# Kernel tuning notes

Hardware: AMD Instinct MI355X
Metric: run time of the kernel (lower is better)

Reference implementation:

```python
import jax, jax.numpy as jnp
import numpy as np

NUM_SLOTS = 2048
LATENT_DIM = 512
EPS = 1e-12  # torch F.normalize clamps norm at eps


def _l2_normalize(x, axis):
    n = jnp.linalg.norm(x, axis=axis, keepdims=True)
    return x / jnp.maximum(n, EPS)


def setup_inputs() -> dict:
    key = jax.random.key(0)
    k_z, k_m = jax.random.split(key)
    z = jax.random.normal(k_z, (65536, LATENT_DIM), dtype=jnp.float32)
    memory = jax.random.normal(k_m, (NUM_SLOTS, LATENT_DIM), dtype=jnp.float32)
    return {"z": z, "memory": memory}


def reference(z, memory):
    # cosine-similarity attention over memory slots
    z_norm = _l2_normalize(z, axis=1)          # [B, D]
    mem_norm = _l2_normalize(memory, axis=1)   # [N, D]
    attn = jax.nn.softmax(z_norm @ mem_norm.T, axis=1)  # [B, N]
    z_hat = attn @ memory                      # [B, D] (unnormalized memory, as in source)
    return (z_hat, attn)
```

## Files before the change

### kernel.cpp

```cpp
#include <hip/hip_runtime.h>

#define NSLOTS 2048
#define DIM    512

typedef __bf16 bf16x8 __attribute__((ext_vector_type(8)));
typedef float  f32x4  __attribute__((ext_vector_type(4)));
typedef unsigned short us4 __attribute__((ext_vector_type(4)));
typedef unsigned short us8 __attribute__((ext_vector_type(8)));

typedef const __attribute__((address_space(1))) unsigned* gp_t;
typedef __attribute__((address_space(3))) unsigned* sp_t;

__device__ __forceinline__ void gl16(const void* g, void* l) {
    __builtin_amdgcn_global_load_lds((gp_t)g, (sp_t)l, 16, 0, 0);
}

__device__ __forceinline__ unsigned short f2bf(float f) {
    unsigned u = __builtin_bit_cast(unsigned, f);
    u = (u + 0x7FFFu + ((u >> 16) & 1u)) >> 16;
    return (unsigned short)u;
}
__device__ __forceinline__ float bf2f(unsigned short u) {
    unsigned v = ((unsigned)u) << 16;
    return __builtin_bit_cast(float, v);
}

__global__ __launch_bounds__(512) void prep_kernel(const float* __restrict__ mem,
                                                   unsigned short* __restrict__ memN,
                                                   unsigned short* __restrict__ memT) {
    __shared__ unsigned short T[32][516];
    const int tid = threadIdx.x;
    const int sl  = tid >> 4;
    const int c16 = tid & 15;
    const int n   = blockIdx.x * 32 + sl;
    const f32x4* row = (const f32x4*)(mem + (size_t)n * DIM);
    f32x4 v[8];
    float s = 0.f;
    #pragma unroll
    for (int j = 0; j < 8; ++j) {
        v[j] = row[c16*8 + j];
        s += v[j][0]*v[j][0] + v[j][1]*v[j][1] + v[j][2]*v[j][2] + v[j][3]*v[j][3];
    }
    #pragma unroll
    for (int off = 1; off < 16; off <<= 1) s += __shfl_xor(s, off);
    const float rn = 1.0f / fmaxf(sqrtf(s), 1e-12f);
    #pragma unroll
    for (int j = 0; j < 8; ++j) {
        us4 p, q;
        #pragma unroll
        for (int e = 0; e < 4; ++e) { p[e] = f2bf(v[j][e] * rn); q[e] = f2bf(v[j][e]); }
        *(us4*)(memN + (size_t)n * DIM + c16*32 + j*4) = p;
        *(us4*)(&T[sl][c16*32 + j*4]) = q;
    }
    __syncthreads();
    {
        const int c4 = tid & 3;
        #pragma unroll
        for (int i = 0; i < 4; ++i) {
            const int dd = i*128 + (tid >> 2);
            us8 g;
            #pragma unroll
            for (int j = 0; j < 8; ++j) g[j] = T[c4*8 + j][dd];
            *(us8*)(memT + (size_t)dd * NSLOTS + blockIdx.x*32 + c4*8) = g;
        }
    }
}

__global__ __launch_bounds__(512) void k1_kernel(const float* __restrict__ z,
                                                 const unsigned short* __restrict__ memN,
                                                 float* attnB,
                                                 float* __restrict__ sums) {
    __shared__ char As[2][8192];
    __shared__ char Bs[2][16384];
    __shared__ float wsums[4][64];
    const int tid  = threadIdx.x;
    const int wid  = tid >> 6;
    const int lane = tid & 63;
    const int l16  = lane & 15;
    const int l4   = lane >> 4;
    const int m    = wid >> 2, n = wid & 3;
    const size_t rowbase = (size_t)blockIdx.x * 64;
    const int r  = tid >> 3;
    const int c8 = tid & 7;
    const int aoff = r*128 + ((c8*16) ^ ((r & 7) << 4));

    us8 a[8];
    {
        const f32x4* zr = (const f32x4*)(z + (rowbase + r) * DIM);
        f32x4 va[8], vb[8];
        float s = 0.f;
        #pragma unroll
        for (int j = 0; j < 8; ++j) {
            va[j] = __builtin_nontemporal_load(zr + c8*2 + j*16);
            vb[j] = __builtin_nontemporal_load(zr + c8*2 + 1 + j*16);
            s += va[j][0]*va[j][0] + va[j][1]*va[j][1] + va[j][2]*va[j][2] + va[j][3]*va[j][3]
               + vb[j][0]*vb[j][0] + vb[j][1]*vb[j][1] + vb[j][2]*vb[j][2] + vb[j][3]*vb[j][3];
        }
        s += __shfl_xor(s, 1); s += __shfl_xor(s, 2); s += __shfl_xor(s, 4);
        const float rn = 1.0f / fmaxf(sqrtf(s), 1e-12f);
        #pragma unroll
        for (int j = 0; j < 8; ++j) {
            us8 p;
            #pragma unroll
            for (int e = 0; e < 4; ++e) { p[e] = f2bf(va[j][e] * rn); p[e + 4] = f2bf(vb[j][e] * rn); }
            a[j] = p;
        }
    }

    auto stageB = [&](int buf, int t) {
        const int c = t >> 3, ks = t & 7;
        #pragma unroll
        for (int i = 0; i < 2; ++i) {
            const int f = (i*8 + wid)*64 + lane, br = f >> 3, g = f & 7;
            const char* src = (const char*)memN + (size_t)(c*128 + br) * 1024 + ks*128
                            + ((g*16) ^ ((br & 7) << 4));
            gl16(src, &Bs[buf][(i*8 + wid)*1024]);
        }
    };

    const f32x4 zeroV = {0.f, 0.f, 0.f, 0.f};
    f32x4 acc[2][2];
    #pragma unroll
    for (int mt = 0; mt < 2; ++mt)
        #pragma unroll
        for (int nt = 0; nt < 2; ++nt) acc[mt][nt] = zeroV;
    float psum[2][4];
    #pragma unroll
    for (int mt = 0; mt < 2; ++mt)
        #pragma unroll
        for (int rr = 0; rr < 4; ++rr) psum[mt][rr] = 0.f;

    *(us8*)(&As[0][aoff]) = a[0];
    stageB(0, 0);
    __syncthreads();

    for (int c = 0; c < 16; ++c) {
        #pragma unroll
        for (int ks = 0; ks < 8; ++ks) {
            const int t = c*8 + ks;
            if (t < 127) {
                *(us8*)(&As[(t + 1) & 1][aoff]) = a[(ks + 1) & 7];
                stageB((t + 1) & 1, t + 1);
            }
            const char* Ab = (const char*)As[t & 1];
            const char* Bb = (const char*)Bs[t & 1];
            #pragma unroll
            for (int kk = 0; kk < 2; ++kk) {
                bf16x8 af[2];
                #pragma unroll
                for (int mt = 0; mt < 2; ++mt) {
                    const int ar = m*32 + mt*16 + l16;
                    af[mt] = *(const bf16x8*)(Ab + ar*128 + ((kk*64 + l4*16) ^ ((ar & 7) << 4)));
                }
                #pragma unroll
                for (int nt = 0; nt < 2; ++nt) {
                    const int br = n*32 + nt*16 + l16;
                    bf16x8 b = *(const bf16x8*)(Bb + br*128 + ((kk*64 + l4*16) ^ ((br & 7) << 4)));
                    acc[0][nt] = __builtin_amdgcn_mfma_f32_16x16x32_bf16(af[0], b, acc[0][nt], 0, 0, 0);
                    acc[1][nt] = __builtin_amdgcn_mfma_f32_16x16x32_bf16(af[1], b, acc[1][nt], 0, 0, 0);
                }
            }
            __syncthreads();
            if (ks == 7) {
                char* Pl = (char*)Bs[t & 1];
                #pragma unroll
                for (int mt = 0; mt < 2; ++mt)
                    #pragma unroll
                    for (int nt = 0; nt < 2; ++nt)
                        #pragma unroll
                        for (int rr = 0; rr < 4; ++rr) {
                            const float e = __expf(acc[mt][nt][rr]);
                            psum[mt][rr] += e;
                            const int row = m*32 + mt*16 + l4*4 + rr;
                            const int sl  = n*32 + nt*16 + l16;
                            *(unsigned short*)(Pl + row*256 + (((sl >> 3) * 16) ^ ((row & 7) << 4)) + (sl & 7)*2) = f2bf(e);
                            acc[mt][nt][rr] = 0.f;
                        }
                __syncthreads();
                {
                    const int prow = tid >> 3, g8 = tid & 7;
                    char* gdst = (char*)attnB + (rowbase + prow) * 8192 + 4096 + c*256;
                    #pragma unroll
                    for (int h = 0; h < 2; ++h) {
                        us8 pv = *(const us8*)(Pl + prow*256 + (((g8 + h*8)*16) ^ ((prow & 7) << 4)));
                        __builtin_nontemporal_store(pv, (us8*)(gdst + (g8 + h*8)*16));
                    }
                }
                __syncthreads();
            }
        }
    }

    #pragma unroll
    for (int mt = 0; mt < 2; ++mt)
        #pragma unroll
        for (int rr = 0; rr < 4; ++rr) {
            #pragma unroll
            for (int off = 1; off < 16; off <<= 1) psum[mt][rr] += __shfl_xor(psum[mt][rr], off);
        }
    if (l16 == 0) {
        #pragma unroll
        for (int mt = 0; mt < 2; ++mt)
            #pragma unroll
            for (int rr = 0; rr < 4; ++rr)
                wsums[n][m*32 + mt*16 + l4*4 + rr] = psum[mt][rr];
    }
    __syncthreads();
    if (tid < 64) sums[rowbase + tid] = wsums[0][tid] + wsums[1][tid] + wsums[2][tid] + wsums[3][tid];
}

__global__ __launch_bounds__(512, 4) void k2_kernel(const unsigned short* __restrict__ memT,
                                                    const float* __restrict__ sums,
                                                    float* __restrict__ zhat,
                                                    float* attnB) {
    __shared__ char ab[2][8192];
    __shared__ char bb[2][16384];
    __shared__ float rsums[64];
    const int tid  = threadIdx.x;
    const int wid  = tid >> 6;
    const int lane = tid & 63;
    const int l16  = lane & 15;
    const int l4   = lane >> 4;
    const int m    = wid >> 2, n = wid & 3;
    const size_t rowbase = (size_t)blockIdx.x * 64;
    const char* attnRd = (const char*)attnB;

    auto stageA = [&](int buf, int ks) {
        const int f = wid*64 + lane, ar = f >> 3, g = f & 7;
        const char* src = attnRd + (rowbase + ar) * 8192 + 4096 + ks*128
                        + ((g*16) ^ ((ar & 7) << 4));
        gl16(src, &ab[buf][0] + wid*1024);
    };
    auto stageB = [&](int buf, int ks, int nb) {
        #pragma unroll
        for (int i = 0; i < 2; ++i) {
            const int f = (i*8 + wid)*64 + lane, dr = f >> 3, g = f & 7;
            const char* src = (const char*)memT + (size_t)(nb*128 + dr) * 4096 + ks*128
                            + ((g*16) ^ ((dr & 7) << 4));
            gl16(src, &bb[buf][0] + (i*8 + wid)*1024);
        }
    };

    if (tid < 64) rsums[tid] = 1.0f / sums[rowbase + tid];

    const f32x4 zeroV = {0.f, 0.f, 0.f, 0.f};
    f32x4 acc[4][2][2];
    #pragma unroll
    for (int nb = 0; nb < 4; ++nb)
        #pragma unroll
        for (int mt = 0; mt < 2; ++mt)
            #pragma unroll
            for (int nt = 0; nt < 2; ++nt) acc[nb][mt][nt] = zeroV;

    stageA(0, 0);
    stageB(0, 0, 0);
    __syncthreads();

    for (int ks = 0; ks < 32; ++ks) {
        #pragma unroll
        for (int nb = 0; nb < 4; ++nb) {
            const int u = ks*4 + nb;
            if (nb < 3) stageB((u + 1) & 1, ks, nb + 1);
            else if (ks < 31) { stageA((ks + 1) & 1, ks + 1); stageB((u + 1) & 1, ks + 1, 0); }
            const char* Ab = (const char*)&ab[ks & 1][0];
            const char* Bb = (const char*)&bb[u & 1][0];
            if (nb == 0) {
                const int prow = tid >> 3;
                const int g = tid & 7;
                const float sc = rsums[prow];
                us8 pv = *(const us8*)(Ab + prow*128 + ((g*16) ^ ((prow & 7) << 4)));
                f32x4 o0, o1;
                #pragma unroll
                for (int e = 0; e < 4; ++e) { o0[e] = bf2f(pv[e]) * sc; o1[e] = bf2f(pv[e + 4]) * sc; }
                float* dst = attnB + (rowbase + prow) * NSLOTS + ks*64 + g*8;
                __builtin_nontemporal_store(o0, (f32x4*)dst);
                __builtin_nontemporal_store(o1, (f32x4*)(dst + 4));
            }
            #pragma unroll
            for (int kk = 0; kk < 2; ++kk) {
                bf16x8 af[2];
                #pragma unroll
                for (int mt = 0; mt < 2; ++mt) {
                    const int ar = m*32 + mt*16 + l16;
                    af[mt] = *(const bf16x8*)(Ab + ar*128 + ((kk*64 + l4*16) ^ ((ar & 7) << 4)));
                }
                #pragma unroll
                for (int nt = 0; nt < 2; ++nt) {
                    const int dr = n*32 + nt*16 + l16;
                    bf16x8 b = *(const bf16x8*)(Bb + dr*128 + ((kk*64 + l4*16) ^ ((dr & 7) << 4)));
                    acc[nb][0][nt] = __builtin_amdgcn_mfma_f32_16x16x32_bf16(af[0], b, acc[nb][0][nt], 0, 0, 0);
                    acc[nb][1][nt] = __builtin_amdgcn_mfma_f32_16x16x32_bf16(af[1], b, acc[nb][1][nt], 0, 0, 0);
                }
            }
            __syncthreads();
        }
    }

    #pragma unroll
    for (int nb = 0; nb < 4; ++nb)
        #pragma unroll
        for (int mt = 0; mt < 2; ++mt)
            #pragma unroll
            for (int rr = 0; rr < 4; ++rr) {
                const int row = m*32 + mt*16 + l4*4 + rr;
                const float rs = rsums[row];
                float* zr = zhat + (rowbase + row) * DIM + nb*128 + n*32 + l16;
                __builtin_nontemporal_store(acc[nb][mt][0][rr] * rs, zr);
                __builtin_nontemporal_store(acc[nb][mt][1][rr] * rs, zr + 16);
            }
}

extern "C" void kernel_launch(void* const* d_in, const int* in_sizes, int n_in,
                              void* d_out, int out_size, void* d_ws, size_t ws_size,
                              hipStream_t stream) {
    const float* zin = (const float*)d_in[0];
    const float* mem = (const float*)d_in[1];
    const int B = in_sizes[0] / DIM;
    unsigned short* memN = (unsigned short*)d_ws;
    unsigned short* memT = memN + (size_t)NSLOTS * DIM;
    float* sums = (float*)(memT + (size_t)NSLOTS * DIM);
    float* zhat = (float*)d_out;
    float* attn = zhat + (size_t)B * DIM;
    prep_kernel<<<NSLOTS / 32, 512, 0, stream>>>(mem, memN, memT);
    k1_kernel<<<B / 64, 512, 0, stream>>>(zin, memN, attn, sums);
    k2_kernel<<<B / 64, 512, 0, stream>>>(memT, sums, zhat, attn);
}
```

Before: 490.9 us.

## Triple-buffer B tiles with partial vmcnt waits in both GEMM kernels

Both GEMM kernels move from double to triple buffering of the B operand in LDS and prefetch two stages ahead. Full __syncthreads waits are replaced with explicit s_waitcnt vmcnt(N) barriers, so outstanding global-to-LDS loads for later stages can stay in flight across iterations. k1 also declares launch_bounds occupancy 4. The aim is to hide global load latency behind the MFMA work, at the cost of more LDS per block and fragile hand-counted wait values.

```diff
diff --git a/kernel.cpp b/kernel.cpp
--- a/kernel.cpp
+++ b/kernel.cpp
@@ -24,6 +24,20 @@
     unsigned v = ((unsigned)u) << 16;
     return __builtin_bit_cast(float, v);
 }
+
+#define WAIT_BAR(N)                                                        \
+    __builtin_amdgcn_sched_barrier(0);                                     \
+    asm volatile("s_waitcnt vmcnt(" #N ") lgkmcnt(0)" ::: "memory");       \
+    __builtin_amdgcn_sched_barrier(0);                                     \
+    __builtin_amdgcn_s_barrier();                                          \
+    __builtin_amdgcn_sched_barrier(0);
+
+#define LGKM_BAR()                                                         \
+    __builtin_amdgcn_sched_barrier(0);                                     \
+    asm volatile("s_waitcnt lgkmcnt(0)" ::: "memory");                     \
+    __builtin_amdgcn_sched_barrier(0);                                     \
+    __builtin_amdgcn_s_barrier();                                          \
+    __builtin_amdgcn_sched_barrier(0);
 
 __global__ __launch_bounds__(512) void prep_kernel(const float* __restrict__ mem,
                                                    unsigned short* __restrict__ memN,
@@ -66,12 +80,12 @@
     }
 }
 
-__global__ __launch_bounds__(512) void k1_kernel(const float* __restrict__ z,
-                                                 const unsigned short* __restrict__ memN,
-                                                 float* attnB,
-                                                 float* __restrict__ sums) {
+__global__ __launch_bounds__(512, 4) void k1_kernel(const float* __restrict__ z,
+                                                    const unsigned short* __restrict__ memN,
+                                                    float* attnB,
+                                                    float* __restrict__ sums) {
     __shared__ char As[2][8192];
-    __shared__ char Bs[2][16384];
+    __shared__ char Bs[3][16384];
     __shared__ float wsums[4][64];
     const int tid  = threadIdx.x;
     const int wid  = tid >> 6;
@@ -107,14 +121,14 @@
         }
     }
 
-    auto stageB = [&](int buf, int t) {
+    auto stageB = [&](int slot, int t) {
         const int c = t >> 3, ks = t & 7;
         #pragma unroll
         for (int i = 0; i < 2; ++i) {
             const int f = (i*8 + wid)*64 + lane, br = f >> 3, g = f & 7;
             const char* src = (const char*)memN + (size_t)(c*128 + br) * 1024 + ks*128
                             + ((g*16) ^ ((br & 7) << 4));
-            gl16(src, &Bs[buf][(i*8 + wid)*1024]);
+            gl16(src, &Bs[slot][(i*8 + wid)*1024]);
         }
     };
 
@@ -132,18 +146,19 @@
 
     *(us8*)(&As[0][aoff]) = a[0];
     stageB(0, 0);
-    __syncthreads();
-
+    stageB(1, 1);
+    WAIT_BAR(2)
+
+    int rs = 0;
     for (int c = 0; c < 16; ++c) {
         #pragma unroll
         for (int ks = 0; ks < 8; ++ks) {
             const int t = c*8 + ks;
-            if (t < 127) {
-                *(us8*)(&As[(t + 1) & 1][aoff]) = a[(ks + 1) & 7];
-                stageB((t + 1) & 1, t + 1);
-            }
+            const int ws = (rs >= 1) ? (rs - 1) : 2;
+            if (t < 127) *(us8*)(&As[(t + 1) & 1][aoff]) = a[(ks + 1) & 7];
+            if (t < 126) stageB(ws, t + 2);
             const char* Ab = (const char*)As[t & 1];
-            const char* Bb = (const char*)Bs[t & 1];
+            const char* Bb = (const char*)Bs[rs];
             #pragma unroll
             for (int kk = 0; kk < 2; ++kk) {
                 bf16x8 af[2];
@@ -160,9 +175,9 @@
                     acc[1][nt] = __builtin_amdgcn_mfma_f32_16x16x32_bf16(af[1], b, acc[1][nt], 0, 0, 0);
                 }
             }
-            __syncthreads();
             if (ks == 7) {
-                char* Pl = (char*)Bs[t & 1];
+                LGKM_BAR()
+                char* Pl = (char*)Bs[rs];
                 #pragma unroll
                 for (int mt = 0; mt < 2; ++mt)
                     #pragma unroll
@@ -176,7 +191,7 @@
                             *(unsigned short*)(Pl + row*256 + (((sl >> 3) * 16) ^ ((row & 7) << 4)) + (sl & 7)*2) = f2bf(e);
                             acc[mt][nt][rr] = 0.f;
                         }
-                __syncthreads();
+                LGKM_BAR()
                 {
                     const int prow = tid >> 3, g8 = tid & 7;
                     char* gdst = (char*)attnB + (rowbase + prow) * 8192 + 4096 + c*256;
@@ -186,8 +201,10 @@
                         __builtin_nontemporal_store(pv, (us8*)(gdst + (g8 + h*8)*16));
                     }
                 }
-                __syncthreads();
-            }
+            }
+            if (t >= 125) { WAIT_BAR(0) }
+            else         { WAIT_BAR(2) }
+            rs = (rs >= 2) ? 0 : rs + 1;
         }
     }
 
@@ -214,7 +231,7 @@
                                                     float* __restrict__ zhat,
                                                     float* attnB) {
     __shared__ char ab[2][8192];
-    __shared__ char bb[2][16384];
+    __shared__ char bb[3][16384];
     __shared__ float rsums[64];
     const int tid  = threadIdx.x;
     const int wid  = tid >> 6;
@@ -231,13 +248,13 @@
                         + ((g*16) ^ ((ar & 7) << 4));
         gl16(src, &ab[buf][0] + wid*1024);
     };
-    auto stageB = [&](int buf, int ks, int nb) {
+    auto stageB = [&](int slot, int ks, int nb) {
         #pragma unroll
         for (int i = 0; i < 2; ++i) {
             const int f = (i*8 + wid)*64 + lane, dr = f >> 3, g = f & 7;
             const char* src = (const char*)memT + (size_t)(nb*128 + dr) * 4096 + ks*128
                             + ((g*16) ^ ((dr & 7) << 4));
-            gl16(src, &bb[buf][0] + (i*8 + wid)*1024);
+            gl16(src, &bb[slot][(i*8 + wid)*1024]);
         }
     };
 
@@ -254,16 +271,19 @@
 
     stageA(0, 0);
     stageB(0, 0, 0);
-    __syncthreads();
-
+    stageB(1, 0, 1);
+    WAIT_BAR(2)
+
+    int rs = 0;
     for (int ks = 0; ks < 32; ++ks) {
         #pragma unroll
         for (int nb = 0; nb < 4; ++nb) {
             const int u = ks*4 + nb;
-            if (nb < 3) stageB((u + 1) & 1, ks, nb + 1);
-            else if (ks < 31) { stageA((ks + 1) & 1, ks + 1); stageB((u + 1) & 1, ks + 1, 0); }
-            const char* Ab = (const char*)&ab[ks & 1][0];
-            const char* Bb = (const char*)&bb[u & 1][0];
+            const int ws = (rs >= 1) ? (rs - 1) : 2;
+            if (u < 126) stageB(ws, (u + 2) >> 2, (u + 2) & 3);
+            if (nb == 1 && ks < 31) stageA((ks + 1) & 1, ks + 1);
+            const char* Ab = (const char*)ab[ks & 1];
+            const char* Bb = (const char*)bb[rs];
             if (nb == 0) {
                 const int prow = tid >> 3;
                 const int g = tid & 7;
@@ -292,7 +312,10 @@
                     acc[nb][1][nt] = __builtin_amdgcn_mfma_f32_16x16x32_bf16(af[1], b, acc[nb][1][nt], 0, 0, 0);
                 }
             }
-            __syncthreads();
+            if (u >= 124)               { WAIT_BAR(0) }
+            else if (nb == 1 || nb == 2){ WAIT_BAR(3) }
+            else                        { WAIT_BAR(2) }
+            rs = (rs >= 2) ? 0 : rs + 1;
         }
     }
 
@@ -303,10 +326,10 @@
             #pragma unroll
             for (int rr = 0; rr < 4; ++rr) {
                 const int row = m*32 + mt*16 + l4*4 + rr;
-                const float rs = rsums[row];
+                const float rsv = rsums[row];
                 float* zr = zhat + (rowbase + row) * DIM + nb*128 + n*32 + l16;
-                __builtin_nontemporal_store(acc[nb][mt][0][rr] * rs, zr);
-                __builtin_nontemporal_store(acc[nb][mt][1][rr] * rs, zr + 16);
+                __builtin_nontemporal_store(acc[nb][mt][0][rr] * rsv, zr);
+                __builtin_nontemporal_store(acc[nb][mt][1][rr] * rsv, zr + 16);
             }
 }
 
```

Measured after the change: 521.0 us. 1.06x slower.

## Widen N tiles to 256 in both GEMM kernels and enlarge LDS buffers

Applied to the files above, without the earlier changes.

Both GEMM kernels now work on 256-wide B tiles instead of 128, so each wave computes a 32x64 output per step. This halves the number of pipeline steps and barriers and improves reuse of the A fragments. LDS is merged into one 80KB buffer per block, and the softmax row-sum reciprocals are read from global memory instead of shared memory. The larger LDS footprint per block may reduce occupancy, and each wave needs more accumulator registers.

```diff
diff --git a/kernel.cpp b/kernel.cpp
--- a/kernel.cpp
+++ b/kernel.cpp
@@ -66,13 +66,11 @@
     }
 }
 
-__global__ __launch_bounds__(512) void k1_kernel(const float* __restrict__ z,
-                                                 const unsigned short* __restrict__ memN,
-                                                 float* attnB,
-                                                 float* __restrict__ sums) {
-    __shared__ char As[2][8192];
-    __shared__ char Bs[2][16384];
-    __shared__ float wsums[4][64];
+__global__ __launch_bounds__(512, 4) void k1_kernel(const float* __restrict__ z,
+                                                    const unsigned short* __restrict__ memN,
+                                                    float* attnB,
+                                                    float* __restrict__ sums) {
+    __shared__ char lds[81920];
     const int tid  = threadIdx.x;
     const int wid  = tid >> 6;
     const int lane = tid & 63;
@@ -84,6 +82,9 @@
     const int c8 = tid & 7;
     const int aoff = r*128 + ((c8*16) ^ ((r & 7) << 4));
 
+    auto Asb = [&](int b) -> char* { return lds + b*8192; };
+    auto Bsb = [&](int b) -> char* { return lds + 16384 + b*32768; };
+
     us8 a[8];
     {
         const f32x4* zr = (const f32x4*)(z + (rowbase + r) * DIM);
@@ -110,40 +111,40 @@
     auto stageB = [&](int buf, int t) {
         const int c = t >> 3, ks = t & 7;
         #pragma unroll
-        for (int i = 0; i < 2; ++i) {
+        for (int i = 0; i < 4; ++i) {
             const int f = (i*8 + wid)*64 + lane, br = f >> 3, g = f & 7;
-            const char* src = (const char*)memN + (size_t)(c*128 + br) * 1024 + ks*128
+            const char* src = (const char*)memN + (size_t)(c*256 + br) * 1024 + ks*128
                             + ((g*16) ^ ((br & 7) << 4));
-            gl16(src, &Bs[buf][(i*8 + wid)*1024]);
+            gl16(src, Bsb(buf) + (i*8 + wid)*1024);
         }
     };
 
     const f32x4 zeroV = {0.f, 0.f, 0.f, 0.f};
-    f32x4 acc[2][2];
+    f32x4 acc[2][4];
     #pragma unroll
     for (int mt = 0; mt < 2; ++mt)
         #pragma unroll
-        for (int nt = 0; nt < 2; ++nt) acc[mt][nt] = zeroV;
+        for (int nt = 0; nt < 4; ++nt) acc[mt][nt] = zeroV;
     float psum[2][4];
     #pragma unroll
     for (int mt = 0; mt < 2; ++mt)
         #pragma unroll
         for (int rr = 0; rr < 4; ++rr) psum[mt][rr] = 0.f;
 
-    *(us8*)(&As[0][aoff]) = a[0];
+    *(us8*)(Asb(0) + aoff) = a[0];
     stageB(0, 0);
     __syncthreads();
 
-    for (int c = 0; c < 16; ++c) {
+    for (int c = 0; c < 8; ++c) {
         #pragma unroll
         for (int ks = 0; ks < 8; ++ks) {
             const int t = c*8 + ks;
-            if (t < 127) {
-                *(us8*)(&As[(t + 1) & 1][aoff]) = a[(ks + 1) & 7];
+            if (t < 63) {
+                *(us8*)(Asb((t + 1) & 1) + aoff) = a[(ks + 1) & 7];
                 stageB((t + 1) & 1, t + 1);
             }
-            const char* Ab = (const char*)As[t & 1];
-            const char* Bb = (const char*)Bs[t & 1];
+            const char* Ab = Asb(t & 1);
+            const char* Bb = Bsb(t & 1);
             #pragma unroll
             for (int kk = 0; kk < 2; ++kk) {
                 bf16x8 af[2];
@@ -153,8 +154,8 @@
                     af[mt] = *(const bf16x8*)(Ab + ar*128 + ((kk*64 + l4*16) ^ ((ar & 7) << 4)));
                 }
                 #pragma unroll
-                for (int nt = 0; nt < 2; ++nt) {
-                    const int br = n*32 + nt*16 + l16;
+                for (int nt = 0; nt < 4; ++nt) {
+                    const int br = n*64 + nt*16 + l16;
                     bf16x8 b = *(const bf16x8*)(Bb + br*128 + ((kk*64 + l4*16) ^ ((br & 7) << 4)));
                     acc[0][nt] = __builtin_amdgcn_mfma_f32_16x16x32_bf16(af[0], b, acc[0][nt], 0, 0, 0);
                     acc[1][nt] = __builtin_amdgcn_mfma_f32_16x16x32_bf16(af[1], b, acc[1][nt], 0, 0, 0);
@@ -162,28 +163,29 @@
             }
             __syncthreads();
             if (ks == 7) {
-                char* Pl = (char*)Bs[t & 1];
+                char* Pl = Bsb(t & 1);
                 #pragma unroll
                 for (int mt = 0; mt < 2; ++mt)
                     #pragma unroll
-                    for (int nt = 0; nt < 2; ++nt)
+                    for (int nt = 0; nt < 4; ++nt)
                         #pragma unroll
                         for (int rr = 0; rr < 4; ++rr) {
                             const float e = __expf(acc[mt][nt][rr]);
                             psum[mt][rr] += e;
                             const int row = m*32 + mt*16 + l4*4 + rr;
-                            const int sl  = n*32 + nt*16 + l16;
-                            *(unsigned short*)(Pl + row*256 + (((sl >> 3) * 16) ^ ((row & 7) << 4)) + (sl & 7)*2) = f2bf(e);
+                            const int sl  = n*64 + nt*16 + l16;
+                            *(unsigned short*)(Pl + row*512 + (((sl >> 3) * 16) ^ ((row & 7) << 4)) + (sl & 7)*2) = f2bf(e);
                             acc[mt][nt][rr] = 0.f;
                         }
                 __syncthreads();
                 {
                     const int prow = tid >> 3, g8 = tid & 7;
-                    char* gdst = (char*)attnB + (rowbase + prow) * 8192 + 4096 + c*256;
+                    char* gdst = (char*)attnB + (rowbase + prow) * 8192 + 4096 + c*512;
                     #pragma unroll
-                    for (int h = 0; h < 2; ++h) {
-                        us8 pv = *(const us8*)(Pl + prow*256 + (((g8 + h*8)*16) ^ ((prow & 7) << 4)));
-                        __builtin_nontemporal_store(pv, (us8*)(gdst + (g8 + h*8)*16));
+                    for (int h = 0; h < 4; ++h) {
+                        const int G = g8 + h*8;
+                        us8 pv = *(const us8*)(Pl + prow*512 + ((G*16) ^ ((prow & 7) << 4)));
+                        __builtin_nontemporal_store(pv, (us8*)(gdst + G*16));
                     }
                 }
                 __syncthreads();
@@ -191,6 +193,7 @@
         }
     }
 
+    float (*wsums)[64] = (float (*)[64])lds;
     #pragma unroll
     for (int mt = 0; mt < 2; ++mt)
         #pragma unroll
@@ -213,9 +216,7 @@
                                                     const float* __restrict__ sums,
                                                     float* __restrict__ zhat,
                                                     float* attnB) {
-    __shared__ char ab[2][8192];
-    __shared__ char bb[2][16384];
-    __shared__ float rsums[64];
+    __shared__ char lds[81920];
     const int tid  = threadIdx.x;
     const int wid  = tid >> 6;
     const int lane = tid & 63;
@@ -225,32 +226,35 @@
     const size_t rowbase = (size_t)blockIdx.x * 64;
     const char* attnRd = (const char*)attnB;
 
+    auto abb = [&](int b) -> char* { return lds + b*8192; };
+    auto bbb = [&](int b) -> char* { return lds + 16384 + b*32768; };
+
     auto stageA = [&](int buf, int ks) {
         const int f = wid*64 + lane, ar = f >> 3, g = f & 7;
         const char* src = attnRd + (rowbase + ar) * 8192 + 4096 + ks*128
                         + ((g*16) ^ ((ar & 7) << 4));
-        gl16(src, &ab[buf][0] + wid*1024);
+        gl16(src, abb(buf) + wid*1024);
     };
     auto stageB = [&](int buf, int ks, int nb) {
         #pragma unroll
-        for (int i = 0; i < 2; ++i) {
+        for (int i = 0; i < 4; ++i) {
             const int f = (i*8 + wid)*64 + lane, dr = f >> 3, g = f & 7;
-            const char* src = (const char*)memT + (size_t)(nb*128 + dr) * 4096 + ks*128
+            const char* src = (const char*)memT + (size_t)(nb*256 + dr) * 4096 + ks*128
                             + ((g*16) ^ ((dr & 7) << 4));
-            gl16(src, &bb[buf][0] + (i*8 + wid)*1024);
+            gl16(src, bbb(buf) + (i*8 + wid)*1024);
         }
     };
 
-    if (tid < 64) rsums[tid] = 1.0f / sums[rowbase + tid];
+    const float sc_attn = 1.0f / sums[rowbase + (tid >> 3)];
 
     const f32x4 zeroV = {0.f, 0.f, 0.f, 0.f};
-    f32x4 acc[4][2][2];
-    #pragma unroll
-    for (int nb = 0; nb < 4; ++nb)
+    f32x4 acc[2][2][4];
+    #pragma unroll
+    for (int nb = 0; nb < 2; ++nb)
         #pragma unroll
         for (int mt = 0; mt < 2; ++mt)
             #pragma unroll
-            for (int nt = 0; nt < 2; ++nt) acc[nb][mt][nt] = zeroV;
+            for (int dt = 0; dt < 4; ++dt) acc[nb][mt][dt] = zeroV;
 
     stageA(0, 0);
     stageB(0, 0, 0);
@@ -258,20 +262,19 @@
 
     for (int ks = 0; ks < 32; ++ks) {
         #pragma unroll
-        for (int nb = 0; nb < 4; ++nb) {
-            const int u = ks*4 + nb;
-            if (nb < 3) stageB((u + 1) & 1, ks, nb + 1);
+        for (int nb = 0; nb < 2; ++nb) {
+            const int u = ks*2 + nb;
+            if (nb == 0) stageB((u + 1) & 1, ks, 1);
             else if (ks < 31) { stageA((ks + 1) & 1, ks + 1); stageB((u + 1) & 1, ks + 1, 0); }
-            const char* Ab = (const char*)&ab[ks & 1][0];
-            const char* Bb = (const char*)&bb[u & 1][0];
+            const char* Ab = abb(ks & 1);
+            const char* Bb = bbb(u & 1);
             if (nb == 0) {
                 const int prow = tid >> 3;
                 const int g = tid & 7;
-                const float sc = rsums[prow];
                 us8 pv = *(const us8*)(Ab + prow*128 + ((g*16) ^ ((prow & 7) << 4)));
                 f32x4 o0, o1;
                 #pragma unroll
-                for (int e = 0; e < 4; ++e) { o0[e] = bf2f(pv[e]) * sc; o1[e] = bf2f(pv[e + 4]) * sc; }
+                for (int e = 0; e < 4; ++e) { o0[e] = bf2f(pv[e]) * sc_attn; o1[e] = bf2f(pv[e + 4]) * sc_attn; }
                 float* dst = attnB + (rowbase + prow) * NSLOTS + ks*64 + g*8;
                 __builtin_nontemporal_store(o0, (f32x4*)dst);
                 __builtin_nontemporal_store(o1, (f32x4*)(dst + 4));
@@ -285,28 +288,34 @@
                     af[mt] = *(const bf16x8*)(Ab + ar*128 + ((kk*64 + l4*16) ^ ((ar & 7) << 4)));
                 }
                 #pragma unroll
-                for (int nt = 0; nt < 2; ++nt) {
-                    const int dr = n*32 + nt*16 + l16;
+                for (int dt = 0; dt < 4; ++dt) {
+                    const int dr = n*64 + dt*16 + l16;
                     bf16x8 b = *(const bf16x8*)(Bb + dr*128 + ((kk*64 + l4*16) ^ ((dr & 7) << 4)));
-                    acc[nb][0][nt] = __builtin_amdgcn_mfma_f32_16x16x32_bf16(af[0], b, acc[nb][0][nt], 0, 0, 0);
-                    acc[nb][1][nt] = __builtin_amdgcn_mfma_f32_16x16x32_bf16(af[1], b, acc[nb][1][nt], 0, 0, 0);
+                    acc[nb][0][dt] = __builtin_amdgcn_mfma_f32_16x16x32_bf16(af[0], b, acc[nb][0][dt], 0, 0, 0);
+                    acc[nb][1][dt] = __builtin_amdgcn_mfma_f32_16x16x32_bf16(af[1], b, acc[nb][1][dt], 0, 0, 0);
                 }
             }
             __syncthreads();
         }
     }
 
-    #pragma unroll
-    for (int nb = 0; nb < 4; ++nb)
+    float rsv[2][4];
+    #pragma unroll
+    for (int mt = 0; mt < 2; ++mt)
+        #pragma unroll
+        for (int rr = 0; rr < 4; ++rr)
+            rsv[mt][rr] = 1.0f / sums[rowbase + m*32 + mt*16 + l4*4 + rr];
+    #pragma unroll
+    for (int nb = 0; nb < 2; ++nb)
         #pragma unroll
         for (int mt = 0; mt < 2; ++mt)
             #pragma unroll
             for (int rr = 0; rr < 4; ++rr) {
                 const int row = m*32 + mt*16 + l4*4 + rr;
-                const float rs = rsums[row];
-                float* zr = zhat + (rowbase + row) * DIM + nb*128 + n*32 + l16;
-                __builtin_nontemporal_store(acc[nb][mt][0][rr] * rs, zr);
-                __builtin_nontemporal_store(acc[nb][mt][1][rr] * rs, zr + 16);
+                float* zr = zhat + (rowbase + row) * DIM + nb*256 + n*64 + l16;
+                #pragma unroll
+                for (int dt = 0; dt < 4; ++dt)
+                    __builtin_nontemporal_store(acc[nb][mt][dt][rr] * rsv[mt][rr], zr + dt*16);
             }
 }
 
```

Measured after the change: 603.1 us. +22.9%, slower.

## Restructure k2 tiling: halve K-step, 256-wide D tiles, fewer barriers per step

Applied to the files above, without the earlier changes.

The second GEMM kernel (attn @ memory) is retiled. Each K step now covers 32 slots with 64-byte rows instead of 64 slots with 128-byte rows, and the D dimension is split into two 256-wide halves instead of four 128-wide quarters. Each wave now computes 4 d-tiles per A fragment, which gives more reuse of A per B load and halves the number of barriers per slot of work. The per-row reciprocal of the softmax sum is now read straight into registers instead of a shared array, and the launch-bounds occupancy hint is dropped. The costs are more outer iterations, narrower global loads, half the threads idle during A staging, and possible changes in register pressure and occupancy.

```diff
diff --git a/kernel.cpp b/kernel.cpp
--- a/kernel.cpp
+++ b/kernel.cpp
@@ -209,13 +209,12 @@
     if (tid < 64) sums[rowbase + tid] = wsums[0][tid] + wsums[1][tid] + wsums[2][tid] + wsums[3][tid];
 }
 
-__global__ __launch_bounds__(512, 4) void k2_kernel(const unsigned short* __restrict__ memT,
-                                                    const float* __restrict__ sums,
-                                                    float* __restrict__ zhat,
-                                                    float* attnB) {
-    __shared__ char ab[2][8192];
+__global__ __launch_bounds__(512) void k2_kernel(const unsigned short* __restrict__ memT,
+                                                 const float* __restrict__ sums,
+                                                 float* __restrict__ zhat,
+                                                 float* attnB) {
+    __shared__ char ab[2][4096];
     __shared__ char bb[2][16384];
-    __shared__ float rsums[64];
     const int tid  = threadIdx.x;
     const int wid  = tid >> 6;
     const int lane = tid & 63;
@@ -226,87 +225,108 @@
     const char* attnRd = (const char*)attnB;
 
     auto stageA = [&](int buf, int ks) {
-        const int f = wid*64 + lane, ar = f >> 3, g = f & 7;
-        const char* src = attnRd + (rowbase + ar) * 8192 + 4096 + ks*128
-                        + ((g*16) ^ ((ar & 7) << 4));
-        gl16(src, &ab[buf][0] + wid*1024);
+        if (tid < 256) {
+            const int ar = tid >> 2, g = tid & 3;
+            const char* src = attnRd + (rowbase + ar) * 8192 + 4096 + ks*64
+                            + ((g*16) ^ ((ar & 3) << 4));
+            gl16(src, &ab[buf][0] + wid*1024);
+        }
     };
     auto stageB = [&](int buf, int ks, int nb) {
         #pragma unroll
         for (int i = 0; i < 2; ++i) {
-            const int f = (i*8 + wid)*64 + lane, dr = f >> 3, g = f & 7;
-            const char* src = (const char*)memT + (size_t)(nb*128 + dr) * 4096 + ks*128
-                            + ((g*16) ^ ((dr & 7) << 4));
+            const int f = i*512 + tid;
+            const int dr = f >> 2, g = f & 3;
+            const char* src = (const char*)memT + (size_t)(nb*256 + dr) * 4096 + ks*64
+                            + ((g*16) ^ ((dr & 3) << 4));
             gl16(src, &bb[buf][0] + (i*8 + wid)*1024);
         }
     };
 
-    if (tid < 64) rsums[tid] = 1.0f / sums[rowbase + tid];
+    const int scrow = (tid < 256) ? (tid >> 2) : 0;
+    const float sc_attn = 1.0f / sums[rowbase + scrow];
 
     const f32x4 zeroV = {0.f, 0.f, 0.f, 0.f};
-    f32x4 acc[4][2][2];
-    #pragma unroll
-    for (int nb = 0; nb < 4; ++nb)
+    f32x4 acc[2][2][4];
+    #pragma unroll
+    for (int nb = 0; nb < 2; ++nb)
         #pragma unroll
         for (int mt = 0; mt < 2; ++mt)
             #pragma unroll
-            for (int nt = 0; nt < 2; ++nt) acc[nb][mt][nt] = zeroV;
+            for (int dt = 0; dt < 4; ++dt) acc[nb][mt][dt] = zeroV;
 
     stageA(0, 0);
     stageB(0, 0, 0);
     __syncthreads();
 
-    for (int ks = 0; ks < 32; ++ks) {
-        #pragma unroll
-        for (int nb = 0; nb < 4; ++nb) {
-            const int u = ks*4 + nb;
-            if (nb < 3) stageB((u + 1) & 1, ks, nb + 1);
-            else if (ks < 31) { stageA((ks + 1) & 1, ks + 1); stageB((u + 1) & 1, ks + 1, 0); }
-            const char* Ab = (const char*)&ab[ks & 1][0];
-            const char* Bb = (const char*)&bb[u & 1][0];
-            if (nb == 0) {
-                const int prow = tid >> 3;
-                const int g = tid & 7;
-                const float sc = rsums[prow];
-                us8 pv = *(const us8*)(Ab + prow*128 + ((g*16) ^ ((prow & 7) << 4)));
+    for (int ks = 0; ks < 64; ++ks) {
+        const char* Ab = (const char*)ab[ks & 1];
+        {
+            if (ks < 63) stageA((ks + 1) & 1, ks + 1);
+            stageB(1, ks, 1);
+            if (tid < 256) {
+                const int ar = tid >> 2, g = tid & 3;
+                us8 pv = *(const us8*)(Ab + ar*64 + ((g*16) ^ ((ar & 3) << 4)));
                 f32x4 o0, o1;
                 #pragma unroll
-                for (int e = 0; e < 4; ++e) { o0[e] = bf2f(pv[e]) * sc; o1[e] = bf2f(pv[e + 4]) * sc; }
-                float* dst = attnB + (rowbase + prow) * NSLOTS + ks*64 + g*8;
+                for (int e = 0; e < 4; ++e) { o0[e] = bf2f(pv[e]) * sc_attn; o1[e] = bf2f(pv[e + 4]) * sc_attn; }
+                float* dst = attnB + (rowbase + ar) * NSLOTS + ks*32 + g*8;
                 __builtin_nontemporal_store(o0, (f32x4*)dst);
                 __builtin_nontemporal_store(o1, (f32x4*)(dst + 4));
             }
-            #pragma unroll
-            for (int kk = 0; kk < 2; ++kk) {
-                bf16x8 af[2];
-                #pragma unroll
-                for (int mt = 0; mt < 2; ++mt) {
-                    const int ar = m*32 + mt*16 + l16;
-                    af[mt] = *(const bf16x8*)(Ab + ar*128 + ((kk*64 + l4*16) ^ ((ar & 7) << 4)));
-                }
-                #pragma unroll
-                for (int nt = 0; nt < 2; ++nt) {
-                    const int dr = n*32 + nt*16 + l16;
-                    bf16x8 b = *(const bf16x8*)(Bb + dr*128 + ((kk*64 + l4*16) ^ ((dr & 7) << 4)));
-                    acc[nb][0][nt] = __builtin_amdgcn_mfma_f32_16x16x32_bf16(af[0], b, acc[nb][0][nt], 0, 0, 0);
-                    acc[nb][1][nt] = __builtin_amdgcn_mfma_f32_16x16x32_bf16(af[1], b, acc[nb][1][nt], 0, 0, 0);
-                }
+            const char* Bb = (const char*)bb[0];
+            bf16x8 af[2];
+            #pragma unroll
+            for (int mt = 0; mt < 2; ++mt) {
+                const int ar = m*32 + mt*16 + l16;
+                af[mt] = *(const bf16x8*)(Ab + ar*64 + ((l4*16) ^ ((ar & 3) << 4)));
+            }
+            #pragma unroll
+            for (int dt = 0; dt < 4; ++dt) {
+                const int dr = n*64 + dt*16 + l16;
+                bf16x8 b = *(const bf16x8*)(Bb + dr*64 + ((l4*16) ^ ((dr & 3) << 4)));
+                acc[0][0][dt] = __builtin_amdgcn_mfma_f32_16x16x32_bf16(af[0], b, acc[0][0][dt], 0, 0, 0);
+                acc[0][1][dt] = __builtin_amdgcn_mfma_f32_16x16x32_bf16(af[1], b, acc[0][1][dt], 0, 0, 0);
             }
             __syncthreads();
         }
-    }
-
-    #pragma unroll
-    for (int nb = 0; nb < 4; ++nb)
+        {
+            if (ks < 63) stageB(0, ks + 1, 0);
+            const char* Bb = (const char*)bb[1];
+            bf16x8 af[2];
+            #pragma unroll
+            for (int mt = 0; mt < 2; ++mt) {
+                const int ar = m*32 + mt*16 + l16;
+                af[mt] = *(const bf16x8*)(Ab + ar*64 + ((l4*16) ^ ((ar & 3) << 4)));
+            }
+            #pragma unroll
+            for (int dt = 0; dt < 4; ++dt) {
+                const int dr = n*64 + dt*16 + l16;
+                bf16x8 b = *(const bf16x8*)(Bb + dr*64 + ((l4*16) ^ ((dr & 3) << 4)));
+                acc[1][0][dt] = __builtin_amdgcn_mfma_f32_16x16x32_bf16(af[0], b, acc[1][0][dt], 0, 0, 0);
+                acc[1][1][dt] = __builtin_amdgcn_mfma_f32_16x16x32_bf16(af[1], b, acc[1][1][dt], 0, 0, 0);
+            }
+            __syncthreads();
+        }
+    }
+
+    float rsv[2][4];
+    #pragma unroll
+    for (int mt = 0; mt < 2; ++mt)
+        #pragma unroll
+        for (int rr = 0; rr < 4; ++rr)
+            rsv[mt][rr] = 1.0f / sums[rowbase + m*32 + mt*16 + l4*4 + rr];
+    #pragma unroll
+    for (int nb = 0; nb < 2; ++nb)
         #pragma unroll
         for (int mt = 0; mt < 2; ++mt)
             #pragma unroll
             for (int rr = 0; rr < 4; ++rr) {
                 const int row = m*32 + mt*16 + l4*4 + rr;
-                const float rs = rsums[row];
-                float* zr = zhat + (rowbase + row) * DIM + nb*128 + n*32 + l16;
-                __builtin_nontemporal_store(acc[nb][mt][0][rr] * rs, zr);
-                __builtin_nontemporal_store(acc[nb][mt][1][rr] * rs, zr + 16);
+                float* zr = zhat + (rowbase + row) * DIM + nb*256 + n*64 + l16;
+                #pragma unroll
+                for (int dt = 0; dt < 4; ++dt)
+                    __builtin_nontemporal_store(acc[nb][mt][dt][rr] * rsv[mt][rr], zr + dt*16);
             }
 }
 
```

Result: slower. 540.6 us (+10.1%).
